# Kernel optimization log

Measured on AMD Instinct MI355X. Metric: run time of the kernel, lower is better.

The kernel has to match this reference:

```python
import jax, jax.numpy as jnp
import numpy as np

VOCAB = 50000
EMB = 128
ENC = 128
B = 256
K = 4            # tree arity
DEPTH = 5        # root at depth 0
N_NODES = (K ** (DEPTH + 1) - 1) // (K - 1)  # 1365, BFS order: children of i are K*i+1..K*i+K


def setup_inputs() -> dict:
    key = jax.random.key(0)
    ks = jax.random.split(key, 9)
    s = 0.05
    return {
        "tokens": jax.random.randint(ks[0], (N_NODES, B), 0, VOCAB, dtype=jnp.int32),
        "emb_table": jax.random.normal(ks[1], (VOCAB, EMB), jnp.float32) * s,
        "W_ih": jax.random.normal(ks[2], (3 * ENC, EMB), jnp.float32) * s,
        "W_hh": jax.random.normal(ks[3], (3 * ENC, ENC), jnp.float32) * s,
        "b_ih": jax.random.normal(ks[4], (3 * ENC,), jnp.float32) * s,
        "b_hh": jax.random.normal(ks[5], (3 * ENC,), jnp.float32) * s,
        "sent_weight": jax.random.normal(ks[6], (ENC, ENC), jnp.float32) * s,
        "sent_bias": jax.random.normal(ks[7], (1, ENC), jnp.float32) * s,
        "context_weight": jax.random.normal(ks[8], (ENC, 1), jnp.float32) * s,
    }


def _gru_step(x, h, W_ih, W_hh, b_ih, b_hh):
    # torch.nn.GRU single step: gates ordered (r, z, n)
    gi = x @ W_ih.T + b_ih
    gh = h @ W_hh.T + b_hh
    i_r, i_z, i_n = jnp.split(gi, 3, axis=-1)
    h_r, h_z, h_n = jnp.split(gh, 3, axis=-1)
    r = jax.nn.sigmoid(i_r + h_r)
    z = jax.nn.sigmoid(i_z + h_z)
    n = jnp.tanh(i_n + r * h_n)
    return (1.0 - z) * n + z * h


def _encode(tokens, emb_table, W_ih, W_hh, b_ih, b_hh, sent_weight, sent_bias, context_weight):
    # bottom-up over levels of a full K-ary tree; vectorized over (nodes-in-level, batch)
    level_starts = [(K ** d - 1) // (K - 1) for d in range(DEPTH + 2)]
    bsz = tokens.shape[1]
    outs = []
    child_h = None  # [n_{d+1}, B, ENC] hiddens of the level below, level-local order
    for d in range(DEPTH, -1, -1):
        s, e = level_starts[d], level_starts[d + 1]
        n_d = e - s
        x = emb_table[tokens[s:e]]  # [n_d, B, EMB]
        if child_h is None:
            h0 = jnp.zeros((n_d, bsz, ENC), x.dtype)  # leaves: no children
        else:
            # children of local node j are rows j*K..j*K+K-1 of child_h
            ch = child_h.reshape(n_d, K, bsz, ENC).transpose(1, 0, 2, 3)  # [K, n_d, B, E]
            u = jnp.tanh(jnp.einsum('knbe,ef->knbf', ch, sent_weight) + sent_bias)
            scores = jnp.tanh(jnp.einsum('knbe,eo->knbo', u, context_weight))[..., 0]  # [K, n_d, B]
            alpha = jax.nn.softmax(scores, axis=0)  # softmax over children, per (node, batch)
            h0 = jnp.einsum('knbe,knb->nbe', ch, alpha)
        hn = _gru_step(x, h0, W_ih, W_hh, b_ih, b_hh)  # [n_d, B, E]
        outs.append(hn)
        child_h = hn
    all_h = jnp.concatenate(outs, axis=0)  # [N_NODES, B, E]
    return jnp.max(all_h, axis=0)  # torch.max(node_list, 0)[0]


def reference(tokens, emb_table, W_ih, W_hh, b_ih, b_hh, sent_weight, sent_bias, context_weight):
    return _encode(tokens, emb_table, W_ih, W_hh, b_ih, b_hh,
                   sent_weight, sent_bias, context_weight)
```

## Files before the change

kernel.cpp:

```cpp
#include <hip/hip_runtime.h>
#include <hip/hip_bf16.h>
#include <math.h>

typedef short s8 __attribute__((ext_vector_type(8)));
typedef float f4 __attribute__((ext_vector_type(4)));
typedef unsigned short ushort_t;

__device__ __forceinline__ float fexp2f(float x) { return __builtin_amdgcn_exp2f(x); }
__device__ __forceinline__ float frcpf(float x)  { return __builtin_amdgcn_rcpf(x); }
__device__ __forceinline__ float sigf(float x) {
    return frcpf(1.f + fexp2f(x * -1.44269504f));
}
__device__ __forceinline__ float tanh_f(float x) {
    float e = fexp2f(x * 2.88539008f);
    return 1.f - 2.f * frcpf(e + 1.f);
}
__device__ __forceinline__ unsigned pk2(float a, float b) {
    __hip_bfloat162 r = __float22bfloat162_rn(make_float2(a, b));
    return *(unsigned*)&r;
}
__device__ __forceinline__ float b2f(ushort_t b) {
    return __uint_as_float(((unsigned)b) << 16);
}
__device__ __forceinline__ ushort_t f2b(float f) {
    unsigned u = __float_as_uint(f);
    u = (u + 0x7FFF + ((u >> 16) & 1)) >> 16;
    return (ushort_t)u;
}

#define EMB_N   6400000
#define W_N     49152
#define SW_N    16384
#define CVT_N   (EMB_N + 2 * W_N + SW_N)

__global__ __launch_bounds__(256) void cvt_kernel(
    const float* __restrict__ emb, const float* __restrict__ wih,
    const float* __restrict__ whh, const float* __restrict__ sw,
    ushort_t* __restrict__ embb, ushort_t* __restrict__ wihb,
    ushort_t* __restrict__ whhb, ushort_t* __restrict__ swtb)
{
    int i = (blockIdx.x * 256 + threadIdx.x) * 4;
    if (i >= CVT_N) return;
    if (i < EMB_N) {
        float4 v = *(const float4*)(emb + i);
        uint2 o; o.x = pk2(v.x, v.y); o.y = pk2(v.z, v.w);
        *(uint2*)(embb + i) = o;
    } else if (i < EMB_N + W_N) {
        int j = i - EMB_N;
        float4 v = *(const float4*)(wih + j);
        uint2 o; o.x = pk2(v.x, v.y); o.y = pk2(v.z, v.w);
        *(uint2*)(wihb + j) = o;
    } else if (i < EMB_N + 2 * W_N) {
        int j = i - EMB_N - W_N;
        float4 v = *(const float4*)(whh + j);
        uint2 o; o.x = pk2(v.x, v.y); o.y = pk2(v.z, v.w);
        *(uint2*)(whhb + j) = o;
    } else {
        int j = i - EMB_N - 2 * W_N;
        int f = j >> 7, e0 = j & 127;
        uint2 o;
        o.x = pk2(sw[(e0 + 0) * 128 + f], sw[(e0 + 1) * 128 + f]);
        o.y = pk2(sw[(e0 + 2) * 128 + f], sw[(e0 + 3) * 128 + f]);
        *(uint2*)(swtb + j) = o;
    }
}

__global__ __launch_bounds__(512, 2) void leafattn_mfma(
    const int* __restrict__ tokens, const ushort_t* __restrict__ embb,
    const ushort_t* __restrict__ wihb,
    const float* __restrict__ bih, const float* __restrict__ bhh,
    const ushort_t* __restrict__ swt, const float* __restrict__ sb,
    const float* __restrict__ cw,
    ushort_t* __restrict__ h0out, ushort_t* __restrict__ pmaxs)
{
    __shared__ ushort_t xs[128 * 136];
    __shared__ ushort_t hnew[128 * 136];
    __shared__ float scp[8][128];
    __shared__ float sc[128];
    __shared__ float al[4][32];

    const int t = threadIdx.x;
    const int pn = blockIdx.x >> 3;
    const int b0 = (blockIdx.x & 7) * 32;

    {
        int lr = t >> 2, c0 = (t & 3) * 32;
        int node = 4 * pn + (lr >> 5), b = b0 + (lr & 31);
        int tok = tokens[(341 + node) * 256 + b];
        const ushort_t* src = embb + (size_t)tok * 128 + c0;
        ushort_t* dst = &xs[lr * 136 + c0];
        #pragma unroll
        for (int i = 0; i < 4; ++i) *(s8*)(dst + 8 * i) = *(const s8*)(src + 8 * i);
    }

    const int lane = t & 63, w = t >> 6;
    const int quad = lane >> 4, l15 = lane & 15;
    const int gA = w * 16 + l15;
    const int g0 = w * 16 + quad * 4;

    s8 bwi[3][4];
    #pragma unroll
    for (int gm = 0; gm < 3; ++gm) {
        const ushort_t* wp = wihb + (size_t)(gm * 128 + gA) * 128 + quad * 8;
        #pragma unroll
        for (int s = 0; s < 4; ++s) bwi[gm][s] = *(const s8*)(wp + 32 * s);
    }
    float bR[4], bZ[4], biN[4], bhN[4];
    {
        float4 a = *(const float4*)(bih + g0);
        float4 b = *(const float4*)(bhh + g0);
        bR[0] = a.x + b.x; bR[1] = a.y + b.y; bR[2] = a.z + b.z; bR[3] = a.w + b.w;
        float4 c = *(const float4*)(bih + 128 + g0);
        float4 d = *(const float4*)(bhh + 128 + g0);
        bZ[0] = c.x + d.x; bZ[1] = c.y + d.y; bZ[2] = c.z + d.z; bZ[3] = c.w + d.w;
        float4 e = *(const float4*)(bih + 256 + g0);
        float4 f = *(const float4*)(bhh + 256 + g0);
        biN[0] = e.x; biN[1] = e.y; biN[2] = e.z; biN[3] = e.w;
        bhN[0] = f.x; bhN[1] = f.y; bhN[2] = f.z; bhN[3] = f.w;
    }

    __syncthreads();

    #pragma unroll 1
    for (int mt = 0; mt < 8; ++mt) {
        const int row = mt * 16 + l15;
        s8 ax[4];
        const ushort_t* ap = &xs[row * 136 + quad * 8];
        #pragma unroll
        for (int s = 0; s < 4; ++s) ax[s] = *(const s8*)(ap + 32 * s);

        f4 accR = (f4)0.f, accZ = (f4)0.f, accN = (f4)0.f;
        #pragma unroll
        for (int s = 0; s < 4; ++s) {
            accR = __builtin_amdgcn_mfma_f32_16x16x32_bf16(bwi[0][s], ax[s], accR, 0, 0, 0);
            accZ = __builtin_amdgcn_mfma_f32_16x16x32_bf16(bwi[1][s], ax[s], accZ, 0, 0, 0);
            accN = __builtin_amdgcn_mfma_f32_16x16x32_bf16(bwi[2][s], ax[s], accN, 0, 0, 0);
        }
        float hv[4];
        #pragma unroll
        for (int r = 0; r < 4; ++r) {
            float rr = sigf(accR[r] + bR[r]);
            float zz = sigf(accZ[r] + bZ[r]);
            float nn = tanh_f(accN[r] + biN[r] + rr * bhN[r]);
            hv[r] = nn - zz * nn;
        }
        uint2 ov; ov.x = pk2(hv[0], hv[1]); ov.y = pk2(hv[2], hv[3]);
        *(uint2*)&hnew[row * 136 + g0] = ov;
    }
    __syncthreads();

    s8 bsw[4];
    {
        const ushort_t* wp = swt + (size_t)gA * 128 + quad * 8;
        #pragma unroll
        for (int s = 0; s < 4; ++s) bsw[s] = *(const s8*)(wp + 32 * s);
    }
    float sb4[4], cw4[4];
    {
        float4 a = *(const float4*)(sb + g0);
        float4 b = *(const float4*)(cw + g0);
        sb4[0] = a.x; sb4[1] = a.y; sb4[2] = a.z; sb4[3] = a.w;
        cw4[0] = b.x; cw4[1] = b.y; cw4[2] = b.z; cw4[3] = b.w;
    }

    #pragma unroll 1
    for (int mt = 0; mt < 8; ++mt) {
        const int crow = mt * 16 + l15;
        s8 a[4];
        const ushort_t* ap = &hnew[crow * 136 + quad * 8];
        #pragma unroll
        for (int s = 0; s < 4; ++s) a[s] = *(const s8*)(ap + 32 * s);

        f4 acc = (f4)0.f;
        #pragma unroll
        for (int s = 0; s < 4; ++s)
            acc = __builtin_amdgcn_mfma_f32_16x16x32_bf16(bsw[s], a[s], acc, 0, 0, 0);

        float part = 0.f;
        #pragma unroll
        for (int r = 0; r < 4; ++r)
            part += tanh_f(acc[r] + sb4[r]) * cw4[r];
        part += __shfl_xor(part, 16);
        part += __shfl_xor(part, 32);
        if (quad == 0) scp[w][crow] = part;
    }
    __syncthreads();

    if (t < 128) {
        float s = 0.f;
        #pragma unroll
        for (int ww = 0; ww < 8; ++ww) s += scp[ww][t];
        sc[t] = tanh_f(s);
    }
    __syncthreads();

    if (t < 32) {
        float s0 = sc[t], s1 = sc[32 + t], s2 = sc[64 + t], s3 = sc[96 + t];
        float m = fmaxf(fmaxf(s0, s1), fmaxf(s2, s3));
        float e0 = fexp2f((s0 - m) * 1.44269504f), e1 = fexp2f((s1 - m) * 1.44269504f);
        float e2 = fexp2f((s2 - m) * 1.44269504f), e3 = fexp2f((s3 - m) * 1.44269504f);
        float inv = frcpf(e0 + e1 + e2 + e3);
        al[0][t] = e0 * inv; al[1][t] = e1 * inv; al[2][t] = e2 * inv; al[3][t] = e3 * inv;
    }
    __syncthreads();

    {
        int bl = t >> 4, e0 = (t & 15) * 8;
        float a0 = al[0][bl], a1 = al[1][bl], a2 = al[2][bl], a3 = al[3][bl];
        s8 c0v = *(const s8*)&hnew[(0 * 32 + bl) * 136 + e0];
        s8 c1v = *(const s8*)&hnew[(1 * 32 + bl) * 136 + e0];
        s8 c2v = *(const s8*)&hnew[(2 * 32 + bl) * 136 + e0];
        s8 c3v = *(const s8*)&hnew[(3 * 32 + bl) * 136 + e0];
        float o[8], m[8];
        #pragma unroll
        for (int j = 0; j < 8; ++j) {
            float x0 = b2f((ushort_t)c0v[j]), x1 = b2f((ushort_t)c1v[j]);
            float x2 = b2f((ushort_t)c2v[j]), x3 = b2f((ushort_t)c3v[j]);
            o[j] = a0 * x0 + a1 * x1 + a2 * x2 + a3 * x3;
            m[j] = fmaxf(fmaxf(x0, x1), fmaxf(x2, x3));
        }
        uint4 ovv, mvv;
        ovv.x = pk2(o[0], o[1]); ovv.y = pk2(o[2], o[3]);
        ovv.z = pk2(o[4], o[5]); ovv.w = pk2(o[6], o[7]);
        mvv.x = pk2(m[0], m[1]); mvv.y = pk2(m[2], m[3]);
        mvv.z = pk2(m[4], m[5]); mvv.w = pk2(m[6], m[7]);
        size_t rh = ((size_t)pn * 256 + b0 + bl) * 128 + e0;
        *(uint4*)(h0out + rh) = ovv;
        size_t rp = ((size_t)(b0 + bl) * 320 + pn) * 128 + e0;
        *(uint4*)(pmaxs + rp) = mvv;
    }
}

__global__ __launch_bounds__(512, 2) void gru_mfma(
    const int* __restrict__ tokens, const ushort_t* __restrict__ embb,
    const ushort_t* __restrict__ wihb, const ushort_t* __restrict__ whhb,
    const float* __restrict__ bih, const float* __restrict__ bhh,
    const ushort_t* __restrict__ h0buf, ushort_t* __restrict__ hbuf,
    int lvl_start)
{
    __shared__ ushort_t xs[128 * 136];
    __shared__ ushort_t hs[128 * 136];

    const int t = threadIdx.x;
    const int base = blockIdx.x * 128;

    {
        int rl = t >> 2, c0 = (t & 3) * 32;
        int row = base + rl;
        int tok = tokens[(lvl_start + (row >> 8)) * 256 + (row & 255)];
        const ushort_t* src = embb + (size_t)tok * 128 + c0;
        ushort_t* dst = &xs[rl * 136 + c0];
        #pragma unroll
        for (int i = 0; i < 4; ++i) *(s8*)(dst + 8 * i) = *(const s8*)(src + 8 * i);
        const ushort_t* hsrc = h0buf + (size_t)row * 128 + c0;
        ushort_t* hdst = &hs[rl * 136 + c0];
        #pragma unroll
        for (int i = 0; i < 4; ++i) *(s8*)(hdst + 8 * i) = *(const s8*)(hsrc + 8 * i);
    }

    const int lane = t & 63, w = t >> 6;
    const int quad = lane >> 4, l15 = lane & 15;
    const int gA = w * 16 + l15;
    const int g0 = w * 16 + quad * 4;

    s8 bwi[3][4], bwh[3][4];
    #pragma unroll
    for (int gm = 0; gm < 3; ++gm) {
        const ushort_t* wp = wihb + (size_t)(gm * 128 + gA) * 128 + quad * 8;
        #pragma unroll
        for (int s = 0; s < 4; ++s) bwi[gm][s] = *(const s8*)(wp + 32 * s);
        const ushort_t* wp2 = whhb + (size_t)(gm * 128 + gA) * 128 + quad * 8;
        #pragma unroll
        for (int s = 0; s < 4; ++s) bwh[gm][s] = *(const s8*)(wp2 + 32 * s);
    }

    float bR[4], bZ[4], biN[4], bhN[4];
    {
        float4 a = *(const float4*)(bih + g0);
        float4 b = *(const float4*)(bhh + g0);
        bR[0] = a.x + b.x; bR[1] = a.y + b.y; bR[2] = a.z + b.z; bR[3] = a.w + b.w;
        float4 c = *(const float4*)(bih + 128 + g0);
        float4 d = *(const float4*)(bhh + 128 + g0);
        bZ[0] = c.x + d.x; bZ[1] = c.y + d.y; bZ[2] = c.z + d.z; bZ[3] = c.w + d.w;
        float4 e = *(const float4*)(bih + 256 + g0);
        float4 f = *(const float4*)(bhh + 256 + g0);
        biN[0] = e.x; biN[1] = e.y; biN[2] = e.z; biN[3] = e.w;
        bhN[0] = f.x; bhN[1] = f.y; bhN[2] = f.z; bhN[3] = f.w;
    }

    __syncthreads();

    #pragma unroll 1
    for (int mt = 0; mt < 8; ++mt) {
        const int row = mt * 16 + l15;
        s8 ax[4], ah[4];
        {
            const ushort_t* ap = &xs[row * 136 + quad * 8];
            #pragma unroll
            for (int s = 0; s < 4; ++s) ax[s] = *(const s8*)(ap + 32 * s);
            const ushort_t* hp = &hs[row * 136 + quad * 8];
            #pragma unroll
            for (int s = 0; s < 4; ++s) ah[s] = *(const s8*)(hp + 32 * s);
        }

        f4 accR = (f4)0.f, accZ = (f4)0.f, accN = (f4)0.f, accNh = (f4)0.f;
        #pragma unroll
        for (int s = 0; s < 4; ++s) {
            accR = __builtin_amdgcn_mfma_f32_16x16x32_bf16(bwi[0][s], ax[s], accR, 0, 0, 0);
            accZ = __builtin_amdgcn_mfma_f32_16x16x32_bf16(bwi[1][s], ax[s], accZ, 0, 0, 0);
            accN = __builtin_amdgcn_mfma_f32_16x16x32_bf16(bwi[2][s], ax[s], accN, 0, 0, 0);
        }
        #pragma unroll
        for (int s = 0; s < 4; ++s) {
            accR  = __builtin_amdgcn_mfma_f32_16x16x32_bf16(bwh[0][s], ah[s], accR, 0, 0, 0);
            accZ  = __builtin_amdgcn_mfma_f32_16x16x32_bf16(bwh[1][s], ah[s], accZ, 0, 0, 0);
            accNh = __builtin_amdgcn_mfma_f32_16x16x32_bf16(bwh[2][s], ah[s], accNh, 0, 0, 0);
        }

        float h0v[4];
        {
            short4 h04 = *(const short4*)&hs[row * 136 + g0];
            h0v[0] = b2f((ushort_t)h04.x); h0v[1] = b2f((ushort_t)h04.y);
            h0v[2] = b2f((ushort_t)h04.z); h0v[3] = b2f((ushort_t)h04.w);
        }
        float hv[4];
        #pragma unroll
        for (int r = 0; r < 4; ++r) {
            float rr = sigf(accR[r] + bR[r]);
            float zz = sigf(accZ[r] + bZ[r]);
            float nn = tanh_f(accN[r] + biN[r] + rr * (accNh[r] + bhN[r]));
            hv[r] = nn + zz * (h0v[r] - nn);
        }
        uint2 ov; ov.x = pk2(hv[0], hv[1]); ov.y = pk2(hv[2], hv[3]);
        *(uint2*)(hbuf + (size_t)(base + row) * 128 + g0) = ov;
    }
}

__global__ __launch_bounds__(512, 2) void attnmax_mfma(
    const ushort_t* __restrict__ hch, ushort_t* __restrict__ h0out,
    ushort_t* __restrict__ pmax,
    const ushort_t* __restrict__ swt, const float* __restrict__ sb,
    const float* __restrict__ cw)
{
    __shared__ ushort_t chs[128 * 136];
    __shared__ float scp[8][128];
    __shared__ float sc[128];
    __shared__ float al[4][32];

    const int t = threadIdx.x;
    const int pbase = blockIdx.x * 32;
    const int pnode = pbase >> 8;
    const int b0 = pbase & 255;

    {
        int lr = t >> 2, c0 = (t & 3) * 32;
        int k = lr >> 5, bl = lr & 31;
        const ushort_t* src = hch + ((size_t)(4 * pnode + k) * 256 + b0 + bl) * 128 + c0;
        ushort_t* dst = &chs[lr * 136 + c0];
        #pragma unroll
        for (int i = 0; i < 4; ++i) *(s8*)(dst + 8 * i) = *(const s8*)(src + 8 * i);
    }

    const int lane = t & 63, w = t >> 6;
    const int quad = lane >> 4, l15 = lane & 15;
    const int fA = w * 16 + l15;
    const int f0 = w * 16 + quad * 4;

    s8 bsw[4];
    {
        const ushort_t* wp = swt + (size_t)fA * 128 + quad * 8;
        #pragma unroll
        for (int s = 0; s < 4; ++s) bsw[s] = *(const s8*)(wp + 32 * s);
    }
    float sb4[4], cw4[4];
    {
        float4 a = *(const float4*)(sb + f0);
        float4 b = *(const float4*)(cw + f0);
        sb4[0] = a.x; sb4[1] = a.y; sb4[2] = a.z; sb4[3] = a.w;
        cw4[0] = b.x; cw4[1] = b.y; cw4[2] = b.z; cw4[3] = b.w;
    }
    __syncthreads();

    #pragma unroll 1
    for (int mt = 0; mt < 8; ++mt) {
        const int crow = mt * 16 + l15;
        s8 a[4];
        const ushort_t* ap = &chs[crow * 136 + quad * 8];
        #pragma unroll
        for (int s = 0; s < 4; ++s) a[s] = *(const s8*)(ap + 32 * s);

        f4 acc = (f4)0.f;
        #pragma unroll
        for (int s = 0; s < 4; ++s)
            acc = __builtin_amdgcn_mfma_f32_16x16x32_bf16(bsw[s], a[s], acc, 0, 0, 0);

        float part = 0.f;
        #pragma unroll
        for (int r = 0; r < 4; ++r)
            part += tanh_f(acc[r] + sb4[r]) * cw4[r];
        part += __shfl_xor(part, 16);
        part += __shfl_xor(part, 32);
        if (quad == 0) scp[w][crow] = part;
    }
    __syncthreads();

    if (t < 128) {
        float s = 0.f;
        #pragma unroll
        for (int ww = 0; ww < 8; ++ww) s += scp[ww][t];
        sc[t] = tanh_f(s);
    }
    __syncthreads();

    if (t < 32) {
        float s0 = sc[t], s1 = sc[32 + t], s2 = sc[64 + t], s3 = sc[96 + t];
        float m = fmaxf(fmaxf(s0, s1), fmaxf(s2, s3));
        float e0 = fexp2f((s0 - m) * 1.44269504f), e1 = fexp2f((s1 - m) * 1.44269504f);
        float e2 = fexp2f((s2 - m) * 1.44269504f), e3 = fexp2f((s3 - m) * 1.44269504f);
        float inv = frcpf(e0 + e1 + e2 + e3);
        al[0][t] = e0 * inv; al[1][t] = e1 * inv; al[2][t] = e2 * inv; al[3][t] = e3 * inv;
    }
    __syncthreads();

    {
        int bl = t >> 4, e0 = (t & 15) * 8;
        float a0 = al[0][bl], a1 = al[1][bl], a2 = al[2][bl], a3 = al[3][bl];
        s8 c0v = *(const s8*)&chs[(0 * 32 + bl) * 136 + e0];
        s8 c1v = *(const s8*)&chs[(1 * 32 + bl) * 136 + e0];
        s8 c2v = *(const s8*)&chs[(2 * 32 + bl) * 136 + e0];
        s8 c3v = *(const s8*)&chs[(3 * 32 + bl) * 136 + e0];
        float o[8], m[8];
        #pragma unroll
        for (int j = 0; j < 8; ++j) {
            float x0 = b2f((ushort_t)c0v[j]), x1 = b2f((ushort_t)c1v[j]);
            float x2 = b2f((ushort_t)c2v[j]), x3 = b2f((ushort_t)c3v[j]);
            o[j] = a0 * x0 + a1 * x1 + a2 * x2 + a3 * x3;
            m[j] = fmaxf(fmaxf(x0, x1), fmaxf(x2, x3));
        }
        uint4 ovv, mvv;
        ovv.x = pk2(o[0], o[1]); ovv.y = pk2(o[2], o[3]);
        ovv.z = pk2(o[4], o[5]); ovv.w = pk2(o[6], o[7]);
        mvv.x = pk2(m[0], m[1]); mvv.y = pk2(m[2], m[3]);
        mvv.z = pk2(m[4], m[5]); mvv.w = pk2(m[6], m[7]);
        size_t rh = ((size_t)pnode * 256 + b0 + bl) * 128 + e0;
        *(uint4*)(h0out + rh) = ovv;
        size_t rp = ((size_t)(b0 + bl) * 320 + 256 + pnode) * 128 + e0;
        *(uint4*)(pmax + rp) = mvv;
    }
}

__global__ __launch_bounds__(512, 1) void tail_kernel(
    const int* __restrict__ tokens, const ushort_t* __restrict__ embb,
    const ushort_t* __restrict__ wihb, const ushort_t* __restrict__ whhb,
    const float* __restrict__ bih, const float* __restrict__ bhh,
    const ushort_t* __restrict__ swt, const float* __restrict__ sb,
    const float* __restrict__ cw,
    const ushort_t* __restrict__ h0g,
    const ushort_t* __restrict__ pmax,
    float* __restrict__ out)
{
    __shared__ ushort_t xs[64 * 136];
    __shared__ ushort_t hnew[64 * 136];
    __shared__ ushort_t hs[64 * 136];
    __shared__ float scp[8][64];
    __shared__ float sc[64];
    __shared__ float al[4][16];
    __shared__ float smax[4][128];
    __shared__ float wpart[8][128];

    const int t = threadIdx.x;
    const int bb = blockIdx.x;
    const int lane = t & 63, w = t >> 6;
    const int quad = lane >> 4, l15 = lane & 15;
    const int gA = w * 16 + l15;
    const int g0 = w * 16 + quad * 4;

    s8 bwi[3][4], bwh[3][4];
    #pragma unroll
    for (int gm = 0; gm < 3; ++gm) {
        const ushort_t* wp = wihb + (size_t)(gm * 128 + gA) * 128 + quad * 8;
        #pragma unroll
        for (int s = 0; s < 4; ++s) bwi[gm][s] = *(const s8*)(wp + 32 * s);
        const ushort_t* wp2 = whhb + (size_t)(gm * 128 + gA) * 128 + quad * 8;
        #pragma unroll
        for (int s = 0; s < 4; ++s) bwh[gm][s] = *(const s8*)(wp2 + 32 * s);
    }
    float bR[4], bZ[4], biN[4], bhN[4];
    {
        float4 a = *(const float4*)(bih + g0);
        float4 b = *(const float4*)(bhh + g0);
        bR[0] = a.x + b.x; bR[1] = a.y + b.y; bR[2] = a.z + b.z; bR[3] = a.w + b.w;
        float4 c = *(const float4*)(bih + 128 + g0);
        float4 d = *(const float4*)(bhh + 128 + g0);
        bZ[0] = c.x + d.x; bZ[1] = c.y + d.y; bZ[2] = c.z + d.z; bZ[3] = c.w + d.w;
        float4 e = *(const float4*)(bih + 256 + g0);
        float4 f = *(const float4*)(bhh + 256 + g0);
        biN[0] = e.x; biN[1] = e.y; biN[2] = e.z; biN[3] = e.w;
        bhN[0] = f.x; bhN[1] = f.y; bhN[2] = f.z; bhN[3] = f.w;
    }
    s8 bsw[4];
    {
        const ushort_t* wp = swt + (size_t)gA * 128 + quad * 8;
        #pragma unroll
        for (int s = 0; s < 4; ++s) bsw[s] = *(const s8*)(wp + 32 * s);
    }
    float sb4[4], cw4[4];
    {
        float4 a = *(const float4*)(sb + g0);
        float4 b = *(const float4*)(cw + g0);
        sb4[0] = a.x; sb4[1] = a.y; sb4[2] = a.z; sb4[3] = a.w;
        cw4[0] = b.x; cw4[1] = b.y; cw4[2] = b.z; cw4[3] = b.w;
    }

    float vmax = -INFINITY;

    const int nodesA[4] = {64, 16, 4, 1};
    const int tok0A[4]  = {21, 5, 1, 0};

    #pragma unroll 1
    for (int L = 0; L < 4; ++L) {
        const int nodes = nodesA[L], tok0 = tok0A[L];
        const int R = (nodes < 16) ? 16 : nodes;
        const int mts = R >> 4;

        {
            int lr = t >> 3, c0 = (t & 7) * 16;
            if (lr < R) {
                int n = min(lr, nodes - 1);
                int tok = tokens[(tok0 + n) * 256 + bb];
                const ushort_t* src = embb + (size_t)tok * 128 + c0;
                ushort_t* dst = &xs[lr * 136 + c0];
                *(s8*)(dst)     = *(const s8*)(src);
                *(s8*)(dst + 8) = *(const s8*)(src + 8);
                if (L == 0) {
                    const ushort_t* hsrc = h0g + ((size_t)n * 256 + bb) * 128 + c0;
                    ushort_t* hdst = &hs[lr * 136 + c0];
                    *(s8*)(hdst)     = *(const s8*)(hsrc);
                    *(s8*)(hdst + 8) = *(const s8*)(hsrc + 8);
                }
            }
        }
        __syncthreads();

        for (int mt = 0; mt < mts; ++mt) {
            const int row = mt * 16 + l15;
            const int hr = min(row, nodes - 1);
            s8 ax[4], ah[4];
            {
                const ushort_t* ap = &xs[row * 136 + quad * 8];
                #pragma unroll
                for (int s = 0; s < 4; ++s) ax[s] = *(const s8*)(ap + 32 * s);
                const ushort_t* hp = &hs[hr * 136 + quad * 8];
                #pragma unroll
                for (int s = 0; s < 4; ++s) ah[s] = *(const s8*)(hp + 32 * s);
            }
            f4 accR = (f4)0.f, accZ = (f4)0.f, accN = (f4)0.f, accNh = (f4)0.f;
            #pragma unroll
            for (int s = 0; s < 4; ++s) {
                accR = __builtin_amdgcn_mfma_f32_16x16x32_bf16(bwi[0][s], ax[s], accR, 0, 0, 0);
                accZ = __builtin_amdgcn_mfma_f32_16x16x32_bf16(bwi[1][s], ax[s], accZ, 0, 0, 0);
                accN = __builtin_amdgcn_mfma_f32_16x16x32_bf16(bwi[2][s], ax[s], accN, 0, 0, 0);
            }
            #pragma unroll
            for (int s = 0; s < 4; ++s) {
                accR  = __builtin_amdgcn_mfma_f32_16x16x32_bf16(bwh[0][s], ah[s], accR, 0, 0, 0);
                accZ  = __builtin_amdgcn_mfma_f32_16x16x32_bf16(bwh[1][s], ah[s], accZ, 0, 0, 0);
                accNh = __builtin_amdgcn_mfma_f32_16x16x32_bf16(bwh[2][s], ah[s], accNh, 0, 0, 0);
            }
            float h0v[4];
            {
                short4 h04 = *(const short4*)&hs[hr * 136 + g0];
                h0v[0] = b2f((ushort_t)h04.x); h0v[1] = b2f((ushort_t)h04.y);
                h0v[2] = b2f((ushort_t)h04.z); h0v[3] = b2f((ushort_t)h04.w);
            }
            float hv[4];
            #pragma unroll
            for (int r = 0; r < 4; ++r) {
                float rr = sigf(accR[r] + bR[r]);
                float zz = sigf(accZ[r] + bZ[r]);
                float nn = tanh_f(accN[r] + biN[r] + rr * (accNh[r] + bhN[r]));
                hv[r] = nn + zz * (h0v[r] - nn);
            }
            uint2 ov; ov.x = pk2(hv[0], hv[1]); ov.y = pk2(hv[2], hv[3]);
            *(uint2*)&hnew[row * 136 + g0] = ov;
        }
        __syncthreads();

        {
            int col = t & 127, g = t >> 7;
            for (int r = g; r < R; r += 4)
                vmax = fmaxf(vmax, b2f(hnew[r * 136 + col]));
        }

        if (L < 3) {
            for (int mt = 0; mt < mts; ++mt) {
                const int crow = mt * 16 + l15;
                s8 a[4];
                const ushort_t* ap = &hnew[crow * 136 + quad * 8];
                #pragma unroll
                for (int s = 0; s < 4; ++s) a[s] = *(const s8*)(ap + 32 * s);
                f4 acc = (f4)0.f;
                #pragma unroll
                for (int s = 0; s < 4; ++s)
                    acc = __builtin_amdgcn_mfma_f32_16x16x32_bf16(bsw[s], a[s], acc, 0, 0, 0);
                float part = 0.f;
                #pragma unroll
                for (int r = 0; r < 4; ++r)
                    part += tanh_f(acc[r] + sb4[r]) * cw4[r];
                part += __shfl_xor(part, 16);
                part += __shfl_xor(part, 32);
                if (quad == 0) scp[w][crow] = part;
            }
            __syncthreads();
            if (t < R) {
                float s = 0.f;
                #pragma unroll
                for (int g = 0; g < 8; ++g) s += scp[g][t];
                sc[t] = tanh_f(s);
            }
            __syncthreads();
            const int P = nodes >> 2;
            if (t < P) {
                float s0 = sc[4 * t + 0], s1 = sc[4 * t + 1];
                float s2 = sc[4 * t + 2], s3 = sc[4 * t + 3];
                float m = fmaxf(fmaxf(s0, s1), fmaxf(s2, s3));
                float e0 = fexp2f((s0 - m) * 1.44269504f);
                float e1 = fexp2f((s1 - m) * 1.44269504f);
                float e2 = fexp2f((s2 - m) * 1.44269504f);
                float e3 = fexp2f((s3 - m) * 1.44269504f);
                float inv = frcpf(e0 + e1 + e2 + e3);
                al[0][t] = e0 * inv; al[1][t] = e1 * inv;
                al[2][t] = e2 * inv; al[3][t] = e3 * inv;
            }
            __syncthreads();
            if (t < 16 * P) {
                int bl = t >> 4, e0 = (t & 15) * 8;
                float a0 = al[0][bl], a1 = al[1][bl], a2 = al[2][bl], a3 = al[3][bl];
                s8 c0v = *(const s8*)&hnew[(4 * bl + 0) * 136 + e0];
                s8 c1v = *(const s8*)&hnew[(4 * bl + 1) * 136 + e0];
                s8 c2v = *(const s8*)&hnew[(4 * bl + 2) * 136 + e0];
                s8 c3v = *(const s8*)&hnew[(4 * bl + 3) * 136 + e0];
                float o[8];
                #pragma unroll
                for (int j = 0; j < 8; ++j) {
                    o[j] = a0 * b2f((ushort_t)c0v[j]) + a1 * b2f((ushort_t)c1v[j])
                         + a2 * b2f((ushort_t)c2v[j]) + a3 * b2f((ushort_t)c3v[j]);
                }
                uint4 ovv;
                ovv.x = pk2(o[0], o[1]); ovv.y = pk2(o[2], o[3]);
                ovv.z = pk2(o[4], o[5]); ovv.w = pk2(o[6], o[7]);
                *(uint4*)&hs[bl * 136 + e0] = ovv;
            }
            __syncthreads();
        }
    }

    smax[t >> 7][t & 127] = vmax;

    {
        int cg = t & 15;
        int ck = t >> 4;
        const ushort_t* base = pmax + (size_t)bb * 320 * 128 + cg * 8;
        float v8[8];
        #pragma unroll
        for (int j = 0; j < 8; ++j) v8[j] = -INFINITY;
        for (int s = ck; s < 320; s += 32) {
            s8 c = *(const s8*)(base + (size_t)s * 128);
            #pragma unroll
            for (int j = 0; j < 8; ++j) v8[j] = fmaxf(v8[j], b2f((ushort_t)c[j]));
        }
        #pragma unroll
        for (int j = 0; j < 8; ++j) {
            v8[j] = fmaxf(v8[j], __shfl_xor(v8[j], 16));
            v8[j] = fmaxf(v8[j], __shfl_xor(v8[j], 32));
        }
        if (lane < 16) {
            #pragma unroll
            for (int j = 0; j < 8; ++j) wpart[w][lane * 8 + j] = v8[j];
        }
    }
    __syncthreads();

    if (t < 128) {
        float m = wpart[0][t];
        #pragma unroll
        for (int ww = 1; ww < 8; ++ww) m = fmaxf(m, wpart[ww][t]);
        float own = fmaxf(fmaxf(smax[0][t], smax[1][t]),
                          fmaxf(smax[2][t], smax[3][t]));
        out[(size_t)bb * 128 + t] = fmaxf(m, own);
    }
}

extern "C" void kernel_launch(void* const* d_in, const int* in_sizes, int n_in,
                              void* d_out, int out_size, void* d_ws, size_t ws_size,
                              hipStream_t stream)
{
    const int*   tokens = (const int*)d_in[0];
    const float* emb    = (const float*)d_in[1];
    const float* Wih    = (const float*)d_in[2];
    const float* Whh    = (const float*)d_in[3];
    const float* bih    = (const float*)d_in[4];
    const float* bhh    = (const float*)d_in[5];
    const float* SW     = (const float*)d_in[6];
    const float* sb     = (const float*)d_in[7];
    const float* cw     = (const float*)d_in[8];
    float* out = (float*)d_out;

    ushort_t* embb = (ushort_t*)d_ws;
    ushort_t* wihb = embb + (size_t)EMB_N;
    ushort_t* whhb = wihb + W_N;
    ushort_t* swtb = whhb + W_N;
    ushort_t* h4   = swtb + SW_N;
    ushort_t* h0_4 = h4 + (size_t)256 * 32768;
    ushort_t* h0_3 = h0_4 + (size_t)256 * 32768;
    ushort_t* pmax = h0_3 + (size_t)64 * 32768;

    cvt_kernel<<<(CVT_N / 4 + 255) / 256, 256, 0, stream>>>(
        emb, Wih, Whh, SW, embb, wihb, whhb, swtb);

    leafattn_mfma<<<2048, 512, 0, stream>>>(
        tokens, embb, wihb, bih, bhh, swtb, sb, cw, h0_4, pmax);

    gru_mfma<<<512, 512, 0, stream>>>(
        tokens, embb, wihb, whhb, bih, bhh, h0_4, h4, 85);
    attnmax_mfma<<<512, 512, 0, stream>>>(h4, h0_3, pmax, swtb, sb, cw);

    tail_kernel<<<256, 512, 0, stream>>>(
        tokens, embb, wihb, whhb, bih, bhh, swtb, sb, cw,
        h0_3, pmax, out);
}
```

Before: 214.6 us.

## Precompute leaf GRU per vocabulary entry and gather, fuse gate reciprocals

```diff
diff --git a/kernel.cpp b/kernel.cpp
--- a/kernel.cpp
+++ b/kernel.cpp
@@ -65,29 +65,19 @@
     }
 }
 
-__global__ __launch_bounds__(512, 2) void leafattn_mfma(
-    const int* __restrict__ tokens, const ushort_t* __restrict__ embb,
-    const ushort_t* __restrict__ wihb,
+__global__ __launch_bounds__(512, 2) void leafgru_mfma(
+    const ushort_t* __restrict__ embb, const ushort_t* __restrict__ wihb,
     const float* __restrict__ bih, const float* __restrict__ bhh,
-    const ushort_t* __restrict__ swt, const float* __restrict__ sb,
-    const float* __restrict__ cw,
-    ushort_t* __restrict__ h0out, ushort_t* __restrict__ pmaxs)
+    ushort_t* __restrict__ hleaf)
 {
     __shared__ ushort_t xs[128 * 136];
-    __shared__ ushort_t hnew[128 * 136];
-    __shared__ float scp[8][128];
-    __shared__ float sc[128];
-    __shared__ float al[4][32];
 
     const int t = threadIdx.x;
-    const int pn = blockIdx.x >> 3;
-    const int b0 = (blockIdx.x & 7) * 32;
+    const int base = blockIdx.x * 128;
 
     {
         int lr = t >> 2, c0 = (t & 3) * 32;
-        int node = 4 * pn + (lr >> 5), b = b0 + (lr & 31);
-        int tok = tokens[(341 + node) * 256 + b];
-        const ushort_t* src = embb + (size_t)tok * 128 + c0;
+        const ushort_t* src = embb + (size_t)(base + lr) * 128 + c0;
         ushort_t* dst = &xs[lr * 136 + c0];
         #pragma unroll
         for (int i = 0; i < 4; ++i) *(s8*)(dst + 8 * i) = *(const s8*)(src + 8 * i);
@@ -139,15 +129,48 @@
         float hv[4];
         #pragma unroll
         for (int r = 0; r < 4; ++r) {
-            float rr = sigf(accR[r] + bR[r]);
-            float zz = sigf(accZ[r] + bZ[r]);
-            float nn = tanh_f(accN[r] + biN[r] + rr * bhN[r]);
-            hv[r] = nn - zz * nn;
+            float G = fexp2f((accR[r] + bR[r]) * -1.44269504f);
+            float rr = frcpf(1.f + G);
+            float an = accN[r] + biN[r] + rr * bhN[r];
+            float E = fexp2f(an * 2.88539008f);
+            float F = fexp2f((accZ[r] + bZ[r]) * -1.44269504f);
+            float d = frcpf((E + 1.f) * (1.f + F));
+            hv[r] = (E - 1.f) * F * d;
         }
         uint2 ov; ov.x = pk2(hv[0], hv[1]); ov.y = pk2(hv[2], hv[3]);
-        *(uint2*)&hnew[row * 136 + g0] = ov;
-    }
-    __syncthreads();
+        *(uint2*)(hleaf + (size_t)(base + row) * 128 + g0) = ov;
+    }
+}
+
+__global__ __launch_bounds__(512, 2) void leafattn_mfma(
+    const int* __restrict__ tokens, const ushort_t* __restrict__ hleaf,
+    const ushort_t* __restrict__ swt, const float* __restrict__ sb,
+    const float* __restrict__ cw,
+    ushort_t* __restrict__ h0out, ushort_t* __restrict__ pmaxs)
+{
+    __shared__ ushort_t xs[128 * 136];
+    __shared__ float scp[8][128];
+    __shared__ float sc[128];
+    __shared__ float al[4][32];
+
+    const int t = threadIdx.x;
+    const int pn = blockIdx.x >> 3;
+    const int b0 = (blockIdx.x & 7) * 32;
+
+    {
+        int lr = t >> 2, c0 = (t & 3) * 32;
+        int node = 4 * pn + (lr >> 5), b = b0 + (lr & 31);
+        int tok = tokens[(341 + node) * 256 + b];
+        const ushort_t* src = hleaf + (size_t)tok * 128 + c0;
+        ushort_t* dst = &xs[lr * 136 + c0];
+        #pragma unroll
+        for (int i = 0; i < 4; ++i) *(s8*)(dst + 8 * i) = *(const s8*)(src + 8 * i);
+    }
+
+    const int lane = t & 63, w = t >> 6;
+    const int quad = lane >> 4, l15 = lane & 15;
+    const int gA = w * 16 + l15;
+    const int g0 = w * 16 + quad * 4;
 
     s8 bsw[4];
     {
@@ -162,12 +185,13 @@
         sb4[0] = a.x; sb4[1] = a.y; sb4[2] = a.z; sb4[3] = a.w;
         cw4[0] = b.x; cw4[1] = b.y; cw4[2] = b.z; cw4[3] = b.w;
     }
+    __syncthreads();
 
     #pragma unroll 1
     for (int mt = 0; mt < 8; ++mt) {
         const int crow = mt * 16 + l15;
         s8 a[4];
-        const ushort_t* ap = &hnew[crow * 136 + quad * 8];
+        const ushort_t* ap = &xs[crow * 136 + quad * 8];
         #pragma unroll
         for (int s = 0; s < 4; ++s) a[s] = *(const s8*)(ap + 32 * s);
 
@@ -207,10 +231,10 @@
     {
         int bl = t >> 4, e0 = (t & 15) * 8;
         float a0 = al[0][bl], a1 = al[1][bl], a2 = al[2][bl], a3 = al[3][bl];
-        s8 c0v = *(const s8*)&hnew[(0 * 32 + bl) * 136 + e0];
-        s8 c1v = *(const s8*)&hnew[(1 * 32 + bl) * 136 + e0];
-        s8 c2v = *(const s8*)&hnew[(2 * 32 + bl) * 136 + e0];
-        s8 c3v = *(const s8*)&hnew[(3 * 32 + bl) * 136 + e0];
+        s8 c0v = *(const s8*)&xs[(0 * 32 + bl) * 136 + e0];
+        s8 c1v = *(const s8*)&xs[(1 * 32 + bl) * 136 + e0];
+        s8 c2v = *(const s8*)&xs[(2 * 32 + bl) * 136 + e0];
+        s8 c3v = *(const s8*)&xs[(3 * 32 + bl) * 136 + e0];
         float o[8], m[8];
         #pragma unroll
         for (int j = 0; j < 8; ++j) {
@@ -326,10 +350,13 @@
         float hv[4];
         #pragma unroll
         for (int r = 0; r < 4; ++r) {
-            float rr = sigf(accR[r] + bR[r]);
-            float zz = sigf(accZ[r] + bZ[r]);
-            float nn = tanh_f(accN[r] + biN[r] + rr * (accNh[r] + bhN[r]));
-            hv[r] = nn + zz * (h0v[r] - nn);
+            float G = fexp2f((accR[r] + bR[r]) * -1.44269504f);
+            float rr = frcpf(1.f + G);
+            float an = accN[r] + biN[r] + rr * (accNh[r] + bhN[r]);
+            float E = fexp2f(an * 2.88539008f);
+            float F = fexp2f((accZ[r] + bZ[r]) * -1.44269504f);
+            float d = frcpf((E + 1.f) * (1.f + F));
+            hv[r] = ((E - 1.f) * F + h0v[r] * (E + 1.f)) * d;
         }
         uint2 ov; ov.x = pk2(hv[0], hv[1]); ov.y = pk2(hv[2], hv[3]);
         *(uint2*)(hbuf + (size_t)(base + row) * 128 + g0) = ov;
@@ -714,12 +741,15 @@
     ushort_t* h0_4 = h4 + (size_t)256 * 32768;
     ushort_t* h0_3 = h0_4 + (size_t)256 * 32768;
     ushort_t* pmax = h0_3 + (size_t)64 * 32768;
+    ushort_t* hleaf = h4;
 
     cvt_kernel<<<(CVT_N / 4 + 255) / 256, 256, 0, stream>>>(
         emb, Wih, Whh, SW, embb, wihb, whhb, swtb);
 
+    leafgru_mfma<<<392, 512, 0, stream>>>(embb, wihb, bih, bhh, hleaf);
+
     leafattn_mfma<<<2048, 512, 0, stream>>>(
-        tokens, embb, wihb, bih, bhh, swtb, sb, cw, h0_4, pmax);
+        tokens, hleaf, swtb, sb, cw, h0_4, pmax);
 
     gru_mfma<<<512, 512, 0, stream>>>(
         tokens, embb, wihb, whhb, bih, bhh, h0_4, h4, 85);
```

After: 186.2 us. 1.15x faster.
